# Kernel tuning notes

Measured on AMD Instinct MI355X. Metric: run time of the kernel, lower is better.

## Reference

```python
import jax, jax.numpy as jnp
import numpy as np

# (l, C_l, C_l_TP, C_l_angular) per non-empty l-block of the filter type
FILTER_REPS = [(0, 144, 144, 1), (1, 272, 272, 1), (2, 208, 208, 1), (3, 80, 80, 1), (4, 16, 16, 1)]
FILTER_C = 720      # sum of C_l
FILTER_DIM = 2704   # sum of C_l*(2l+1)
ANG_DIM = 25        # sum of C_l_angular*(2l+1)
DIM_OUT = 52
DIM_IN = 52
Q_OUT, Q_IN, NUM_P = 16, 16, 125
SCALAR_BASIS = 12


def setup_inputs() -> dict:
    key = jax.random.key(0)
    k1, k2, k3, k4, k5 = jax.random.split(key, 5)
    N = Q_OUT * Q_IN * NUM_P
    scalar_kernel_tensor = jax.random.normal(k1, (Q_OUT, Q_IN, NUM_P, SCALAR_BASIS), dtype=jnp.float32)
    angular_kernel_tensor = jax.random.normal(k2, (N, ANG_DIM), dtype=jnp.float32)
    weights = jax.random.normal(k3, (SCALAR_BASIS, FILTER_C), dtype=jnp.float32)
    # TP mixing matrix is a constant sparse buffer (Wigner-3j based); model as sparsified dense
    dense = jax.random.normal(k4, (DIM_OUT * DIM_IN, FILTER_DIM), dtype=jnp.float32)
    mask = jax.random.uniform(k5, (DIM_OUT * DIM_IN, FILTER_DIM)) < 0.05
    TP_mixing = dense * mask.astype(jnp.float32)
    return {"scalar_kernel_tensor": scalar_kernel_tensor,
            "angular_kernel_tensor": angular_kernel_tensor,
            "weights": weights,
            "TP_mixing": TP_mixing}


def mul_scalar_angular(sc, ang):
    # sc: (N, FILTER_C), ang: (N, ANG_DIM) -> (N, FILTER_DIM)
    N = sc.shape[0]
    outs = []
    s = 0
    a = 0
    for (l, C_l, C_l_TP, C_l_ang) in FILTER_REPS:
        m = 2 * l + 1
        dim_ang = C_l_ang * m
        x = (sc[:, s:s + C_l].reshape(N, C_l_ang, C_l_TP, 1)
             * ang[:, a:a + dim_ang].reshape(N, C_l_ang, 1, m))
        outs.append(x.reshape(N, C_l * m))
        s += C_l
        a += dim_ang
    return jnp.concatenate(outs, axis=-1)


def reference(scalar_kernel_tensor, angular_kernel_tensor, weights, TP_mixing):
    N = Q_OUT * Q_IN * NUM_P
    sk = scalar_kernel_tensor.reshape(N, SCALAR_BASIS)
    # combine scalar basis with weights: (N, FILTER_C)
    sc = jnp.einsum('ns,sc->nc', sk, weights / jnp.sqrt(jnp.float32(SCALAR_BASIS)))
    # ragged segment-wise broadcast multiply: (N, FILTER_DIM)
    filt = mul_scalar_angular(sc, angular_kernel_tensor)
    # kernel = (TP_mixing @ filt.T).T == filt @ TP_mixing.T : (N, DIM_OUT*DIM_IN)
    k = filt @ TP_mixing.T
    return k.reshape(Q_OUT, Q_IN, NUM_P, DIM_OUT, DIM_IN)
```

## Files before the change

kernel.cpp:

```cpp
#include <hip/hip_runtime.h>
#include <hip/hip_bf16.h>

#define N_ROWS 32000
#define SB     12
#define FC     720
#define FD     2704
#define OCOLS  2704
#define OPAD   2816
#define ANGD   25
#define PDIM   300
#define KST    320
#define NT     5
#define KP     2720
#define NTV    85
#define GPR    (KP/8)

typedef __attribute__((ext_vector_type(8))) short bf16x8;
typedef __attribute__((ext_vector_type(4))) float f32x4;

__device__ __forceinline__ void gload16(const void* g, void* l) {
    __builtin_amdgcn_global_load_lds(
        (const __attribute__((address_space(1))) void*)g,
        (__attribute__((address_space(3))) void*)l, 16, 0, 0);
}

__device__ __forceinline__ void decode_f(int f, int& c, int& j, int& a) {
    if (f < 144)       { c = f;                         j = 0;            a = 0;  }
    else if (f < 960)  { int t = f - 144;  c = 144 + t/3; j = t - (t/3)*3; a = 1;  }
    else if (f < 2000) { int t = f - 960;  c = 416 + t/5; j = t - (t/5)*5; a = 4;  }
    else if (f < 2560) { int t = f - 2000; c = 624 + t/7; j = t - (t/7)*7; a = 9;  }
    else               { int t = f - 2560; c = 704 + t/9; j = t - (t/9)*9; a = 16; }
}

__global__ void cvt_M(const float* __restrict__ M, __hip_bfloat16* __restrict__ out)
{
    const int g = blockIdx.x * 256 + threadIdx.x;
    if (g >= OPAD * GPR) return;
    const int o = g / GPR;
    const int k = (g - o * GPR) * 8;
    alignas(16) __hip_bfloat16 tmp[8];
    if (o < OCOLS && k + 8 <= FD) {
        const float4* p = (const float4*)(M + (size_t)o * FD + k);
        float4 x0 = p[0], x1 = p[1];
        tmp[0] = __float2bfloat16(x0.x); tmp[1] = __float2bfloat16(x0.y);
        tmp[2] = __float2bfloat16(x0.z); tmp[3] = __float2bfloat16(x0.w);
        tmp[4] = __float2bfloat16(x1.x); tmp[5] = __float2bfloat16(x1.y);
        tmp[6] = __float2bfloat16(x1.z); tmp[7] = __float2bfloat16(x1.w);
    } else {
        #pragma unroll
        for (int u = 0; u < 8; ++u) {
            float v = (o < OCOLS && k + u < FD) ? M[(size_t)o * FD + k + u] : 0.f;
            tmp[u] = __float2bfloat16(v);
        }
    }
    *(bf16x8*)(out + (size_t)o * KP + k) = *(const bf16x8*)tmp;
}

__global__ void build_G(const float* __restrict__ W, __hip_bfloat16* __restrict__ Gt)
{
    const int g = blockIdx.x * 256 + threadIdx.x;
    if (g >= KST * GPR) return;
    const int p  = g / GPR;
    const int f0 = (g - p * GPR) * 8;
    const int s     = p / ANGD;
    const int alpha = p - s * ANGD;
    const float inv = 0.28867513459481288f;
    alignas(16) __hip_bfloat16 tmp[8];
    #pragma unroll
    for (int u = 0; u < 8; ++u) {
        const int f = f0 + u;
        float v = 0.f;
        if (p < PDIM && f < FD) {
            int c, j, a;
            decode_f(f, c, j, a);
            if (alpha == a + j) v = W[s * FC + c] * inv;
        }
        tmp[u] = __float2bfloat16(v);
    }
    *(bf16x8*)(Gt + (size_t)p * KP + f0) = *(const bf16x8*)tmp;
}

__global__ void build_X(const float* __restrict__ sk,
                        const float* __restrict__ ang,
                        __hip_bfloat16* __restrict__ X)
{
    const int idx = blockIdx.x * 256 + threadIdx.x;
    if (idx >= N_ROWS * (KST / 8)) return;
    const int n  = idx / (KST / 8);
    const int p0 = (idx - n * (KST / 8)) * 8;
    const float* skn  = sk  + (size_t)n * SB;
    const float* angn = ang + (size_t)n * ANGD;
    alignas(16) __hip_bfloat16 tmp[8];
    #pragma unroll
    for (int u = 0; u < 8; ++u) {
        const int p = p0 + u;
        float v = 0.f;
        if (p < PDIM) {
            const int s = p / ANGD;
            const int a = p - s * ANGD;
            v = skn[s] * angn[a];
        }
        tmp[u] = __float2bfloat16(v);
    }
    *(bf16x8*)(X + (size_t)n * KST + p0) = *(const bf16x8*)tmp;
}

__global__ __launch_bounds__(256, 4) void gemm_V(
    const __hip_bfloat16* __restrict__ A,
    const __hip_bfloat16* __restrict__ B,
    __hip_bfloat16* __restrict__ V)
{
    __shared__ __align__(1024) char lds[24576];
    char* const bufA = lds;
    char* const bufB = lds + 16384;

    const int tid  = threadIdx.x;
    const int wave = tid >> 6;
    const int lane = tid & 63;

    const int bn = blockIdx.x;
    const int bm = blockIdx.y;
    const size_t arow0 = (size_t)bm * 128;
    const size_t brow0 = (size_t)bn * 64;

    const int wr = wave >> 1;
    const int wc = wave & 1;

    const int lrow2 = lane >> 2;
    const int sslot = (((lane & 3) ^ (lrow2 & 3) ^ ((lane >> 4) & 3))) << 4;

    auto STAGE = [&](int t, int half) {
        char* const la = bufA + half * 8192;
        char* const lb = bufB + half * 4096;
        const char* ga = (const char*)A
            + (arow0 + (size_t)(wave * 16 + lrow2)) * (KP * 2)
            + (size_t)t * 64 + sslot;
        gload16(ga,                         la + wave * 1024);
        gload16(ga + (size_t)64 * (KP * 2), la + 4096 + wave * 1024);
        const char* gb = (const char*)B
            + (brow0 + (size_t)(wave * 16 + lrow2)) * (KP * 2)
            + (size_t)t * 64 + sslot;
        gload16(gb, lb + wave * 1024);
    };

    const int rl   = lane & 15;
    const int koct = lane >> 4;
    const int rslot = ((koct ^ (rl & 3) ^ ((rl >> 2) & 3))) << 4;

    STAGE(0, 0);
    STAGE(1, 1);
    asm volatile("s_waitcnt vmcnt(3)" ::: "memory");
    __builtin_amdgcn_s_barrier();

    f32x4 acc[4][2] = {};

    for (int t = 0; t < NTV; ++t) {
        char* const aC = bufA + (t & 1) * 8192;
        char* const bC = bufB + (t & 1) * 4096;

        bf16x8 af[4], bfr[2];
        #pragma unroll
        for (int m = 0; m < 4; ++m) {
            const int r = wr * 64 + m * 16 + rl;
            af[m] = *(const bf16x8*)(aC + r * 64 + rslot);
        }
        #pragma unroll
        for (int n = 0; n < 2; ++n) {
            const int r = wc * 32 + n * 16 + rl;
            bfr[n] = *(const bf16x8*)(bC + r * 64 + rslot);
        }
        asm volatile("s_waitcnt lgkmcnt(0)" ::: "memory");
        __builtin_amdgcn_sched_barrier(0);
        __builtin_amdgcn_s_barrier();

        if (t + 2 < NTV) STAGE(t + 2, t & 1);

        __builtin_amdgcn_s_setprio(1);
        #pragma unroll
        for (int m = 0; m < 4; ++m)
            #pragma unroll
            for (int n = 0; n < 2; ++n)
                acc[m][n] = __builtin_amdgcn_mfma_f32_16x16x32_bf16(
                    bfr[n], af[m], acc[m][n], 0, 0, 0);
        __builtin_amdgcn_s_setprio(0);
        __builtin_amdgcn_sched_barrier(0);

        if (t < NTV - 2)       asm volatile("s_waitcnt vmcnt(3)" ::: "memory");
        else if (t == NTV - 2) asm volatile("s_waitcnt vmcnt(0)" ::: "memory");
        if (t < NTV - 1) __builtin_amdgcn_s_barrier();
    }

    const int obase = (int)arow0 + wr * 64 + rl;
    const int pbase = (int)brow0 + wc * 32 + koct * 4;
    #pragma unroll
    for (int m = 0; m < 4; ++m) {
        const int orow = obase + m * 16;
        #pragma unroll
        for (int n = 0; n < 2; ++n) {
            const int p = pbase + n * 16;
            alignas(8) __hip_bfloat16 t4[4];
            t4[0] = __float2bfloat16(acc[m][n][0]);
            t4[1] = __float2bfloat16(acc[m][n][1]);
            t4[2] = __float2bfloat16(acc[m][n][2]);
            t4[3] = __float2bfloat16(acc[m][n][3]);
            *(uint2*)(V + (size_t)orow * KST + p) = *(const uint2*)t4;
        }
    }
}

__global__ __launch_bounds__(512, 2) void gemm_bt(
    const __hip_bfloat16* __restrict__ A,
    const __hip_bfloat16* __restrict__ B,
    float* __restrict__ C)
{
    __shared__ __align__(1024) char lds[81920];
    char* const bufA = lds;
    char* const bufB = lds + 16384;
    float* const s_c = (float*)lds;

    const int tid  = threadIdx.x;
    const int wave = tid >> 6;
    const int lane = tid & 63;

    const int bn = blockIdx.x;
    const int bm = blockIdx.y;
    const size_t arow0 = (size_t)bm * 64;
    const size_t brow0 = (size_t)bn * 256;

    const int lrow  = lane >> 3;
    const int lslot = ((lane & 7) ^ (lrow & 7)) << 4;

    auto STAGE = [&](int t, int half) {
        char* const la = bufA + half * 8192;
        char* const lb = bufB + half * 32768;
        const char* ga = (const char*)A
            + (arow0 + (size_t)(wave * 8 + lrow)) * (KST * 2)
            + (size_t)t * 128 + lslot;
        gload16(ga, la + wave * 1024);
        const char* gb = (const char*)B
            + (brow0 + (size_t)(wave * 8 + lrow)) * (KST * 2)
            + (size_t)t * 128 + lslot;
        #pragma unroll
        for (int i = 0; i < 4; ++i)
            gload16(gb + (size_t)(64 * i) * (KST * 2), lb + i * 8192 + wave * 1024);
    };

    const int rl   = lane & 15;
    const int koct = lane >> 4;
    const int sK0 = ((0 * 4 + koct) ^ (lane & 7)) << 4;
    const int sK1 = ((1 * 4 + koct) ^ (lane & 7)) << 4;

    STAGE(0, 0);
    STAGE(1, 1);
    asm volatile("s_waitcnt vmcnt(5)" ::: "memory");
    __builtin_amdgcn_s_barrier();

    f32x4 acc[4][2] = {};

    for (int t = 0; t < NT; ++t) {
        char* const aC = bufA + (t & 1) * 8192;
        char* const bC = bufB + (t & 1) * 32768;

        bf16x8 af[4][2], bfr[2][2];
        #pragma unroll
        for (int m = 0; m < 4; ++m) {
            const int r = m * 16 + rl;
            af[m][0] = *(const bf16x8*)(aC + r * 128 + sK0);
            af[m][1] = *(const bf16x8*)(aC + r * 128 + sK1);
        }
        #pragma unroll
        for (int n = 0; n < 2; ++n) {
            const int r = wave * 32 + n * 16 + rl;
            bfr[n][0] = *(const bf16x8*)(bC + r * 128 + sK0);
            bfr[n][1] = *(const bf16x8*)(bC + r * 128 + sK1);
        }
        asm volatile("s_waitcnt lgkmcnt(0)" ::: "memory");
        __builtin_amdgcn_sched_barrier(0);
        __builtin_amdgcn_s_barrier();

        if (t + 2 < NT) STAGE(t + 2, t & 1);

        __builtin_amdgcn_s_setprio(1);
        #pragma unroll
        for (int ks = 0; ks < 2; ++ks)
            #pragma unroll
            for (int m = 0; m < 4; ++m)
                #pragma unroll
                for (int n = 0; n < 2; ++n)
                    acc[m][n] = __builtin_amdgcn_mfma_f32_16x16x32_bf16(
                        bfr[n][ks], af[m][ks], acc[m][n], 0, 0, 0);
        __builtin_amdgcn_s_setprio(0);
        __builtin_amdgcn_sched_barrier(0);

        if (t < NT - 2)       asm volatile("s_waitcnt vmcnt(5)" ::: "memory");
        else if (t == NT - 2) asm volatile("s_waitcnt vmcnt(0)" ::: "memory");
        if (t < NT - 1) __builtin_amdgcn_s_barrier();
    }

    __syncthreads();
    #pragma unroll
    for (int m = 0; m < 4; ++m) {
        const int row_l = m * 16 + rl;
        #pragma unroll
        for (int n = 0; n < 2; ++n) {
            const int col = wave * 32 + n * 16 + koct * 4;
            *(f32x4*)&s_c[row_l * 260 + col] = acc[m][n];
        }
    }
    __syncthreads();
    #pragma unroll
    for (int rr = 0; rr < 8; ++rr) {
        const int idx = rr * 512 + tid;
        const int row = idx >> 6;
        const int g4  = (idx & 63) * 4;
        if ((int)brow0 + g4 < OCOLS) {
            const f32x4 v = *(const f32x4*)&s_c[row * 260 + g4];
            __builtin_nontemporal_store(v,
                (f32x4*)(C + (size_t)(arow0 + row) * OCOLS + brow0 + g4));
        }
    }
}

extern "C" void kernel_launch(void* const* d_in, const int* in_sizes, int n_in,
                              void* d_out, int out_size, void* d_ws, size_t ws_size,
                              hipStream_t stream)
{
    const float* sk  = (const float*)d_in[0];
    const float* ang = (const float*)d_in[1];
    const float* W   = (const float*)d_in[2];
    const float* TP  = (const float*)d_in[3];
    float* out = (float*)d_out;

    __hip_bfloat16* X   = (__hip_bfloat16*)d_ws;
    __hip_bfloat16* Vb  = X   + (size_t)N_ROWS * KST;
    __hip_bfloat16* TPb = Vb  + (size_t)OPAD * KST;
    __hip_bfloat16* Gt  = TPb + (size_t)OPAD * KP;

    cvt_M<<<(OPAD * GPR + 255) / 256, 256, 0, stream>>>(TP, TPb);
    build_G<<<(KST * GPR + 255) / 256, 256, 0, stream>>>(W, Gt);
    build_X<<<(N_ROWS * (KST / 8) + 255) / 256, 256, 0, stream>>>(sk, ang, X);

    dim3 gridV(KST / 64, OPAD / 128);
    gemm_V<<<gridV, 256, 0, stream>>>(TPb, Gt, Vb);

    dim3 grid(OPAD / 256, N_ROWS / 64);
    gemm_bt<<<grid, 512, 0, stream>>>(X, Vb, out);
}
```

Before: 147.7 us.

## Enlarge final GEMM tile to 256x256 with quarter-stepped pipelined staging

The final GEMM's block tile grows from 64x256 to 256x256 on a 2x4 wave grid. Each wave now holds an 8x4 accumulator array, and the launch becomes a 1D grid of 125*11 blocks. The k-loop is split into four sub-steps that each issue one slice of the next tile's global-to-LDS loads, so loads are spread out and overlap the MFMA work. The epilogue writes back through LDS in four 64-row passes. The aim is higher operand reuse and less redundant B traffic, at the cost of 128KB of LDS, more registers and lower occupancy.

```diff
diff --git a/kernel.cpp b/kernel.cpp
--- a/kernel.cpp
+++ b/kernel.cpp
@@ -213,110 +213,139 @@
     const __hip_bfloat16* __restrict__ B,
     float* __restrict__ C)
 {
-    __shared__ __align__(1024) char lds[81920];
-    char* const bufA = lds;
-    char* const bufB = lds + 16384;
+    __shared__ __align__(1024) char lds[131072];
+    char* const ldsA = lds;
+    char* const ldsB = lds + 65536;
     float* const s_c = (float*)lds;
 
     const int tid  = threadIdx.x;
     const int wave = tid >> 6;
     const int lane = tid & 63;
 
-    const int bn = blockIdx.x;
-    const int bm = blockIdx.y;
-    const size_t arow0 = (size_t)bm * 64;
+    const int wgid = blockIdx.x;
+    const int bm = wgid / 11;
+    const int bn = wgid - bm * 11;
+    const size_t arow0 = (size_t)bm * 256;
     const size_t brow0 = (size_t)bn * 256;
+
+    const int wr = wave >> 2;
+    const int wc = wave & 3;
 
     const int lrow  = lane >> 3;
     const int lslot = ((lane & 7) ^ (lrow & 7)) << 4;
 
-    auto STAGE = [&](int t, int half) {
-        char* const la = bufA + half * 8192;
-        char* const lb = bufB + half * 32768;
-        const char* ga = (const char*)A
-            + (arow0 + (size_t)(wave * 8 + lrow)) * (KST * 2)
-            + (size_t)t * 128 + lslot;
-        gload16(ga, la + wave * 1024);
-        const char* gb = (const char*)B
-            + (brow0 + (size_t)(wave * 8 + lrow)) * (KST * 2)
-            + (size_t)t * 128 + lslot;
-        #pragma unroll
-        for (int i = 0; i < 4; ++i)
-            gload16(gb + (size_t)(64 * i) * (KST * 2), lb + i * 8192 + wave * 1024);
+    auto STAGE = [&](const char* gbase, size_t growbase, int tile, char* lbase) {
+        const char* g0 = gbase + (growbase + (size_t)(wave * 8 + lrow)) * (KST * 2)
+                               + (size_t)tile * 128 + lslot;
+        gload16(g0,                          lbase + wave * 1024);
+        gload16(g0 + (size_t)64 * (KST * 2), lbase + 8192 + wave * 1024);
     };
 
     const int rl   = lane & 15;
     const int koct = lane >> 4;
     const int sK0 = ((0 * 4 + koct) ^ (lane & 7)) << 4;
     const int sK1 = ((1 * 4 + koct) ^ (lane & 7)) << 4;
-
-    STAGE(0, 0);
-    STAGE(1, 1);
-    asm volatile("s_waitcnt vmcnt(5)" ::: "memory");
+    const int arow = wr * 64 + rl;
+    const int brow = (wc & 1) * 64 + rl;
+    const int bhalf = wc >> 1;
+
+    STAGE((const char*)B, brow0 + 0,   0, ldsB + 0);
+    STAGE((const char*)B, brow0 + 128, 0, ldsB + 16384);
+    STAGE((const char*)A, arow0 + 0,   0, ldsA + 0);
+    STAGE((const char*)A, arow0 + 128, 0, ldsA + 16384);
+    STAGE((const char*)B, brow0 + 0,   1, ldsB + 32768);
+    STAGE((const char*)B, brow0 + 128, 1, ldsB + 32768 + 16384);
+    STAGE((const char*)A, arow0 + 0,   1, ldsA + 32768);
+    asm volatile("s_waitcnt vmcnt(6)" ::: "memory");
     __builtin_amdgcn_s_barrier();
 
-    f32x4 acc[4][2] = {};
+    f32x4 acc[8][4] = {};
 
     for (int t = 0; t < NT; ++t) {
-        char* const aC = bufA + (t & 1) * 8192;
-        char* const bC = bufB + (t & 1) * 32768;
-
-        bf16x8 af[4][2], bfr[2][2];
-        #pragma unroll
-        for (int m = 0; m < 4; ++m) {
-            const int r = m * 16 + rl;
-            af[m][0] = *(const bf16x8*)(aC + r * 128 + sK0);
-            af[m][1] = *(const bf16x8*)(aC + r * 128 + sK1);
-        }
-        #pragma unroll
-        for (int n = 0; n < 2; ++n) {
-            const int r = wave * 32 + n * 16 + rl;
-            bfr[n][0] = *(const bf16x8*)(bC + r * 128 + sK0);
-            bfr[n][1] = *(const bf16x8*)(bC + r * 128 + sK1);
-        }
-        asm volatile("s_waitcnt lgkmcnt(0)" ::: "memory");
-        __builtin_amdgcn_sched_barrier(0);
-        __builtin_amdgcn_s_barrier();
-
-        if (t + 2 < NT) STAGE(t + 2, t & 1);
-
-        __builtin_amdgcn_s_setprio(1);
-        #pragma unroll
-        for (int ks = 0; ks < 2; ++ks)
+        char* const aB  = ldsA + (t & 1) * 32768;
+        char* const bB  = ldsB + (t & 1) * 32768;
+        char* const aBn = ldsA + ((t + 1) & 1) * 32768;
+
+        bf16x8 bfr[4][2];
+        #pragma unroll
+        for (int q = 0; q < 4; ++q) {
+            asm volatile("" ::: "memory");
+            __builtin_amdgcn_sched_barrier(0);
+
+            bf16x8 af[2][2];
+            char* ah = aB + (q >> 1) * 16384;
             #pragma unroll
-            for (int m = 0; m < 4; ++m)
+            for (int m = 0; m < 2; ++m) {
+                const int r = arow + (q & 1) * 32 + m * 16;
+                af[m][0] = *(const bf16x8*)(ah + r * 128 + sK0);
+                af[m][1] = *(const bf16x8*)(ah + r * 128 + sK1);
+            }
+            if (q == 0) {
+                char* bh = bB + bhalf * 16384;
                 #pragma unroll
-                for (int n = 0; n < 2; ++n)
-                    acc[m][n] = __builtin_amdgcn_mfma_f32_16x16x32_bf16(
-                        bfr[n][ks], af[m][ks], acc[m][n], 0, 0, 0);
-        __builtin_amdgcn_s_setprio(0);
-        __builtin_amdgcn_sched_barrier(0);
-
-        if (t < NT - 2)       asm volatile("s_waitcnt vmcnt(5)" ::: "memory");
-        else if (t == NT - 2) asm volatile("s_waitcnt vmcnt(0)" ::: "memory");
-        if (t < NT - 1) __builtin_amdgcn_s_barrier();
-    }
-
-    __syncthreads();
+                for (int n = 0; n < 4; ++n) {
+                    bfr[n][0] = *(const bf16x8*)(bh + (brow + n * 16) * 128 + sK0);
+                    bfr[n][1] = *(const bf16x8*)(bh + (brow + n * 16) * 128 + sK1);
+                }
+            }
+
+            if (q == 0 && t + 1 < NT) STAGE((const char*)A, arow0 + 128, t + 1, aBn + 16384);
+            if (q == 1 && t + 2 < NT) STAGE((const char*)B, brow0 + 0,   t + 2, bB + 0);
+            if (q == 2 && t + 2 < NT) STAGE((const char*)B, brow0 + 128, t + 2, bB + 16384);
+            if (q == 3 && t + 2 < NT) STAGE((const char*)A, arow0 + 0,   t + 2, aB + 0);
+
+            __builtin_amdgcn_s_barrier();
+            asm volatile("s_waitcnt lgkmcnt(0)" ::: "memory");
+            __builtin_amdgcn_sched_barrier(0);
+
+            __builtin_amdgcn_s_setprio(1);
+            #pragma unroll
+            for (int ks = 0; ks < 2; ++ks)
+                #pragma unroll
+                for (int m = 0; m < 2; ++m)
+                    #pragma unroll
+                    for (int n = 0; n < 4; ++n)
+                        acc[q * 2 + m][n] = __builtin_amdgcn_mfma_f32_16x16x32_bf16(
+                            bfr[n][ks], af[m][ks], acc[q * 2 + m][n], 0, 0, 0);
+            __builtin_amdgcn_s_setprio(0);
+            __builtin_amdgcn_sched_barrier(0);
+
+            if (q == 3 && t + 1 < NT) {
+                if (t + 1 == NT - 1) asm volatile("s_waitcnt vmcnt(0)" ::: "memory");
+                else                 asm volatile("s_waitcnt vmcnt(6)" ::: "memory");
+            }
+            __builtin_amdgcn_s_barrier();
+        }
+    }
+
     #pragma unroll
-    for (int m = 0; m < 4; ++m) {
-        const int row_l = m * 16 + rl;
-        #pragma unroll
-        for (int n = 0; n < 2; ++n) {
-            const int col = wave * 32 + n * 16 + koct * 4;
-            *(f32x4*)&s_c[row_l * 260 + col] = acc[m][n];
-        }
-    }
-    __syncthreads();
-    #pragma unroll
-    for (int rr = 0; rr < 8; ++rr) {
-        const int idx = rr * 512 + tid;
-        const int row = idx >> 6;
-        const int g4  = (idx & 63) * 4;
-        if ((int)brow0 + g4 < OCOLS) {
-            const f32x4 v = *(const f32x4*)&s_c[row * 260 + g4];
-            __builtin_nontemporal_store(v,
-                (f32x4*)(C + (size_t)(arow0 + row) * OCOLS + brow0 + g4));
+    for (int h = 0; h < 4; ++h) {
+        __syncthreads();
+        if (wr == (h & 1)) {
+            const int qh = (h >> 1) * 2;
+            #pragma unroll
+            for (int qq = 0; qq < 2; ++qq)
+                #pragma unroll
+                for (int m = 0; m < 2; ++m) {
+                    const int row_l = qq * 32 + m * 16 + rl;
+                    #pragma unroll
+                    for (int n = 0; n < 4; ++n) {
+                        const int col = wc * 64 + n * 16 + koct * 4;
+                        *(f32x4*)&s_c[row_l * 260 + col] = acc[(qh + qq) * 2 + m][n];
+                    }
+                }
+        }
+        __syncthreads();
+        #pragma unroll
+        for (int rr = 0; rr < 8; ++rr) {
+            const int idx = rr * 512 + tid;
+            const int row = idx >> 6;
+            const int g4  = (idx & 63) * 4;
+            if ((int)brow0 + g4 < OCOLS) {
+                const f32x4 v = *(const f32x4*)&s_c[row * 260 + g4];
+                __builtin_nontemporal_store(v,
+                    (f32x4*)(C + (size_t)(arow0 + h * 64 + row) * OCOLS + brow0 + g4));
+            }
         }
     }
 }
@@ -343,6 +372,5 @@
     dim3 gridV(KST / 64, OPAD / 128);
     gemm_V<<<gridV, 256, 0, stream>>>(TPb, Gt, Vb);
 
-    dim3 grid(OPAD / 256, N_ROWS / 64);
-    gemm_bt<<<grid, 512, 0, stream>>>(X, Vb, out);
-}
+    gemm_bt<<<125 * 11, 512, 0, stream>>>(X, Vb, out);
+}
```

Result: slower. 160.9 us (+8.9%).
